# Kernel tuning notes

Hardware: AMD Instinct MI355X
Metric: run time of the kernel (lower is better)

The kernel has to match this reference:

```python
import jax, jax.numpy as jnp
import numpy as np

NEG_INF = float(np.finfo(np.float32).min)
B, KLEN, QLEN, KDIM, QDIM, ADIM, H = 2, 2048, 2048, 512, 512, 512, 8
D_K = ADIM // H


def setup_inputs() -> dict:
    key = jax.random.key(0)
    ks = jax.random.split(key, 12)
    s = 0.05  # param init scale
    inp = {
        "key_in": jax.random.normal(ks[0], (B, KLEN, KDIM), jnp.float32),
        "value_in": jax.random.normal(ks[1], (B, KLEN, KDIM), jnp.float32),
        "query_in": jax.random.normal(ks[2], (B, QLEN, QDIM), jnp.float32),
        "Wk": jax.random.normal(ks[3], (KDIM, ADIM), jnp.float32) * s,
        "bk": jax.random.normal(ks[4], (ADIM,), jnp.float32) * s,
        "Wv": jax.random.normal(ks[5], (KDIM, ADIM), jnp.float32) * s,
        "bv": jax.random.normal(ks[6], (ADIM,), jnp.float32) * s,
        "Wq": jax.random.normal(ks[7], (QDIM, ADIM), jnp.float32) * s,
        "bq": jax.random.normal(ks[8], (ADIM,), jnp.float32) * s,
        "Wo": jax.random.normal(ks[9], (ADIM, KDIM), jnp.float32) * s,
        "bo": jax.random.normal(ks[10], (KDIM,), jnp.float32) * s,
    }
    # key-length padding mask, [B, qlen, klen]; 0 = masked
    klens = jnp.array([KLEN, KLEN - 512], jnp.int32)
    valid = (jnp.arange(KLEN)[None, :] < klens[:, None]).astype(jnp.int32)  # [B, klen]
    inp["mask"] = jnp.broadcast_to(valid[:, None, :], (B, QLEN, KLEN))
    return inp


def reference(key_in, value_in, query_in, Wk, bk, Wv, bv, Wq, bq, Wo, bo, mask):
    # projections -> [B, L, H, d_k]
    k = (key_in @ Wk + bk).reshape(B, KLEN, H, D_K)
    v = (value_in @ Wv + bv).reshape(B, KLEN, H, D_K)
    q = (query_in @ Wq + bq).reshape(B, QLEN, H, D_K)
    # scaled dot-product scores [B, H, qlen, klen]
    e = jnp.einsum('bqhd,bkhd->bhqk', q, k) / jnp.sqrt(jnp.float32(D_K))
    e = jnp.where(mask[:, None, :, :] == 0, NEG_INF, e)
    aw = jax.nn.softmax(e, axis=-1)  # dropout p=0.0 -> identity
    cv = jnp.einsum('bhqk,bkhd->bqhd', aw, v).reshape(B, QLEN, ADIM)
    cv = cv @ Wo + bo  # [B, qlen, kdim]
    return cv, aw
```

## Files before the change

kernel.cpp:

```cpp
#include <hip/hip_runtime.h>

typedef short sh8 __attribute__((ext_vector_type(8)));
typedef float fx4 __attribute__((ext_vector_type(4)));
typedef float fl4 __attribute__((ext_vector_type(4)));
typedef unsigned short us4 __attribute__((ext_vector_type(4)));

__device__ __forceinline__ unsigned short f2bf(float f) {
    union { float f; unsigned u; } v; v.f = f;
    unsigned r = v.u + 0x7FFFu + ((v.u >> 16) & 1u);
    return (unsigned short)(r >> 16);
}
__device__ __forceinline__ float EX2(float x) { return __builtin_amdgcn_exp2f(x); }
__device__ __forceinline__ unsigned cvtpk(float a, float b) {
    unsigned r;
    asm("v_cvt_pk_bf16_f32 %0, %1, %2" : "=v"(r) : "v"(a), "v"(b));
    return r;
}
__device__ __forceinline__ void gl16(const unsigned short* g, unsigned short* l) {
    __builtin_amdgcn_global_load_lds(
        (const __attribute__((address_space(1))) unsigned int*)g,
        (__attribute__((address_space(3))) unsigned int*)l, 16, 0, 0);
}

__global__ __launch_bounds__(256) void prep(const float* __restrict__ x0,
                                            const float* __restrict__ x1,
                                            const float* __restrict__ x2,
                                            const float* __restrict__ w0,
                                            const float* __restrict__ w1,
                                            const float* __restrict__ w2,
                                            const float* __restrict__ w3,
                                            const int* __restrict__ mask,
                                            unsigned short* __restrict__ in_bf,
                                            unsigned short* __restrict__ wt,
                                            unsigned long long* __restrict__ mp2) {
    __shared__ float tw[32][33];
    const int bid = blockIdx.x, tid = threadIdx.x;
    if (bid < 1536) {
        const int z = bid >> 9, xb = bid & 511;
        const float* src = z == 0 ? x0 : (z == 1 ? x1 : x2);
        unsigned short* dst = in_bf + (size_t)z * 2097152;
        for (int i = xb * 256 + tid; i < 524288; i += 131072) {
            float4 v = ((const float4*)src)[i];
            ushort4 o;
            o.x = f2bf(v.x); o.y = f2bf(v.y); o.z = f2bf(v.z); o.w = f2bf(v.w);
            ((ushort4*)dst)[i] = o;
        }
    } else if (bid < 2560) {
        const int t = bid - 1536;
        const int z = t >> 8, bx = t & 15, by = (t >> 4) & 15;
        const float* W = z == 0 ? w0 : z == 1 ? w1 : z == 2 ? w2 : w3;
        unsigned short* Wt = wt + (size_t)z * 262144;
        const int tx = tid & 31, ty = tid >> 5;
        #pragma unroll
        for (int i = 0; i < 4; ++i)
            tw[ty + i * 8][tx] = W[(size_t)(by * 32 + ty + i * 8) * 512 + bx * 32 + tx];
        __syncthreads();
        #pragma unroll
        for (int i = 0; i < 4; ++i)
            Wt[(size_t)(bx * 32 + ty + i * 8) * 512 + by * 32 + tx] = f2bf(tw[tx][ty + i * 8]);
    } else {
        const int p = bid - 2560;
        const int b = p >> 3, k = (p & 7) * 256 + tid;
        int v = mask[(size_t)b * 4194304 + k];
        unsigned long long bal = __ballot(v != 0);
        if ((tid & 63) == 0) mp2[b * 32 + (k >> 6)] = bal;
    }
}

template <int MODE>
__global__ __launch_bounds__(256) void gemm_k(const unsigned short* __restrict__ Aall,
                                              const unsigned short* __restrict__ Wtall,
                                              const float* __restrict__ b0,
                                              const float* __restrict__ b1,
                                              const float* __restrict__ b2,
                                              void* __restrict__ outp,
                                              unsigned short* __restrict__ VtB) {
    const int z = blockIdx.z;
    const unsigned short* A  = Aall  + (size_t)z * (4096 * 512);
    const unsigned short* Bt = Wtall + (size_t)z * (512 * 512);
    const float* bias = (MODE == 0) ? (z == 0 ? b0 : (z == 1 ? b1 : b2)) : b0;

    __shared__ __align__(16) unsigned short As[128 * 64];
    __shared__ __align__(16) unsigned short Bs[64 * 64];

    const int tid = threadIdx.x;
    const int wid = tid >> 6, lane = tid & 63, lr = lane & 15, lg = lane >> 4;
    const int wr = wid >> 1, wc = wid & 1;
    const int mblk = blockIdx.x * 128, nblk = blockIdx.y * 64;
    const int r7 = lr & 7;

    fx4 acc[4][2];
    #pragma unroll
    for (int mf = 0; mf < 4; ++mf)
        #pragma unroll
        for (int nf = 0; nf < 2; ++nf)
            #pragma unroll
            for (int j = 0; j < 4; ++j) acc[mf][nf][j] = 0.f;

    for (int kt = 0; kt < 8; ++kt) {
        __syncthreads();
        #pragma unroll
        for (int g = 0; g < 4; ++g) {
            int ci = wid * 256 + g * 64 + lane;
            int r = ci >> 3, c = (ci & 7) ^ (r & 7);
            gl16(A + (size_t)(mblk + r) * 512 + kt * 64 + c * 8, &As[(wid * 256 + g * 64) * 8]);
        }
        #pragma unroll
        for (int g = 0; g < 2; ++g) {
            int ci = wid * 128 + g * 64 + lane;
            int r = ci >> 3, c = (ci & 7) ^ (r & 7);
            gl16(Bt + (size_t)(nblk + r) * 512 + kt * 64 + c * 8, &Bs[(wid * 128 + g * 64) * 8]);
        }
        __syncthreads();
        #pragma unroll
        for (int d = 0; d < 2; ++d) {
            sh8 af[4], bf[2];
            #pragma unroll
            for (int mf = 0; mf < 4; ++mf)
                af[mf] = *(const sh8*)&As[(wr * 64 + mf * 16 + lr) * 64 + (((d * 4 + lg) ^ r7) * 8)];
            #pragma unroll
            for (int nf = 0; nf < 2; ++nf)
                bf[nf] = *(const sh8*)&Bs[(wc * 32 + nf * 16 + lr) * 64 + (((d * 4 + lg) ^ r7) * 8)];
            #pragma unroll
            for (int mf = 0; mf < 4; ++mf)
                #pragma unroll
                for (int nf = 0; nf < 2; ++nf)
                    acc[mf][nf] = __builtin_amdgcn_mfma_f32_16x16x32_bf16(af[mf], bf[nf], acc[mf][nf], 0, 0, 0);
        }
    }

    if (MODE == 0 && z == 1) {
        #pragma unroll
        for (int nf = 0; nf < 2; ++nf) {
            int n = nblk + wc * 32 + nf * 16 + lr;
            float bv = bias[n];
            int h = n >> 6, dd = n & 63;
            #pragma unroll
            for (int mf = 0; mf < 4; ++mf) {
                int m0 = mblk + wr * 64 + mf * 16 + lg * 4;
                int bb = m0 >> 11, lq = m0 & 2047;
                ushort4 o;
                o.x = f2bf(acc[mf][nf][0] + bv);
                o.y = f2bf(acc[mf][nf][1] + bv);
                o.z = f2bf(acc[mf][nf][2] + bv);
                o.w = f2bf(acc[mf][nf][3] + bv);
                *(ushort4*)(VtB + ((size_t)(bb * 8 + h) * 64 + dd) * 2048 + lq) = o;
            }
        }
    } else {
        #pragma unroll
        for (int nf = 0; nf < 2; ++nf) {
            int n = nblk + wc * 32 + nf * 16 + lr;
            float bv = bias[n];
            #pragma unroll
            for (int mf = 0; mf < 4; ++mf) {
                #pragma unroll
                for (int j = 0; j < 4; ++j) {
                    int m = mblk + wr * 64 + mf * 16 + lg * 4 + j;
                    float val = acc[mf][nf][j] + bv;
                    if (MODE == 0) {
                        if (z == 2) val *= 0.180336880f;
                        int bb = m >> 11, lq = m & 2047, h = n >> 6, dd = n & 63;
                        ((unsigned short*)outp)[(size_t)(((z * 2 + bb) * 8 + h) * 2048 + lq) * 64 + dd] = f2bf(val);
                    } else {
                        ((float*)outp)[(size_t)m * 512 + n] = val;
                    }
                }
            }
        }
    }
}

__device__ __forceinline__ void stage_k1(const unsigned short* Kg, unsigned short* sK,
                                         int t, int w, int lane) {
    #pragma unroll
    for (int g = 0; g < 2; ++g) {
        int ci = w * 128 + g * 64 + lane;
        int r = ci >> 3, c = (ci & 7) ^ (r & 7);
        gl16(Kg + (size_t)(t * 64 + r) * 64 + c * 8, sK + (w * 128 + g * 64) * 8);
    }
}
__device__ __forceinline__ void stage_kv(const unsigned short* Kg, const unsigned short* Vg,
                                         unsigned short* sK, unsigned short* sV,
                                         int t, int w, int lane) {
    #pragma unroll
    for (int g = 0; g < 2; ++g) {
        int ci = w * 128 + g * 64 + lane;
        int r = ci >> 3, c = (ci & 7) ^ (r & 7);
        gl16(Kg + (size_t)(t * 64 + r) * 64 + c * 8, sK + (w * 128 + g * 64) * 8);
        gl16(Vg + (size_t)r * 2048 + t * 64 + c * 8, sV + (w * 128 + g * 64) * 8);
    }
}

__global__ __launch_bounds__(256, 2) void attn_fused(const unsigned short* __restrict__ qkv,
                                                     const unsigned short* __restrict__ Vt,
                                                     const unsigned long long* __restrict__ mp2,
                                                     float* __restrict__ aw,
                                                     unsigned short* __restrict__ cv) {
    const int bid = blockIdx.x;
    const int swz = (bid & 7) * 64 + (bid >> 3);
    const int qb = swz & 31, bh = swz >> 5;
    const int b = bh >> 3, h = bh & 7;
    const unsigned short* Kg = qkv + (size_t)bh * 131072;
    const unsigned short* Vg = Vt + (size_t)bh * 131072;
    const unsigned short* Qg = qkv + 2 * 2097152 + (size_t)bh * 131072 + (size_t)qb * 4096;

    __shared__ __align__(16) unsigned short Ks[2][4096];
    __shared__ __align__(16) unsigned short Vs[2][4096];
    __shared__ __align__(16) unsigned short Pb[4096];

    const int tid = threadIdx.x, w = tid >> 6, lane = tid & 63, lr = lane & 15, lg = lane >> 4;
    const int r7 = lr & 7;
    const int q = qb * 64 + w * 16 + lr;

    sh8 qf0 = *(const sh8*)(Qg + (w * 16 + lr) * 64 + lg * 8);
    sh8 qf1 = *(const sh8*)(Qg + (w * 16 + lr) * 64 + 32 + lg * 8);
    unsigned long long mwv = (lane < 32) ? mp2[b * 32 + lane] : 0ull;

    float m_ = -3e38f, l_ = 0.f;
    asm volatile("s_waitcnt vmcnt(0)" ::: "memory");
    stage_k1(Kg, Ks[0], 0, w, lane);
    stage_k1(Kg, Ks[1], 1, w, lane);
    for (int kt = 0; kt < 32; ++kt) {
        if (kt >= 1 && kt <= 30)
            stage_k1(Kg, Ks[(kt + 1) & 1], kt + 1, w, lane);
        if (kt == 31) asm volatile("s_waitcnt vmcnt(0)" ::: "memory");
        else          asm volatile("s_waitcnt vmcnt(2)" ::: "memory");
        asm volatile("s_barrier" ::: "memory");
        unsigned long long mw = __shfl(mwv, kt, 64);
        if (mw != 0ull) {
            const unsigned short* KsB = Ks[kt & 1];
            fx4 accs[4];
            #pragma unroll
            for (int mt = 0; mt < 4; ++mt) {
                sh8 kf0 = *(const sh8*)&KsB[(mt * 16 + lr) * 64 + ((lg ^ r7) * 8)];
                sh8 kf1 = *(const sh8*)&KsB[(mt * 16 + lr) * 64 + (((4 + lg) ^ r7) * 8)];
                fx4 zz; zz[0] = 0.f; zz[1] = 0.f; zz[2] = 0.f; zz[3] = 0.f;
                zz = __builtin_amdgcn_mfma_f32_16x16x32_bf16(kf0, qf0, zz, 0, 0, 0);
                accs[mt] = __builtin_amdgcn_mfma_f32_16x16x32_bf16(kf1, qf1, zz, 0, 0, 0);
            }
            float sv[16], tmax = -3e38f;
            if (mw == ~0ull) {
                #pragma unroll
                for (int mt = 0; mt < 4; ++mt)
                    #pragma unroll
                    for (int j = 0; j < 4; ++j) {
                        float s = accs[mt][j];
                        sv[mt * 4 + j] = s; tmax = fmaxf(tmax, s);
                    }
            } else {
                #pragma unroll
                for (int mt = 0; mt < 4; ++mt)
                    #pragma unroll
                    for (int j = 0; j < 4; ++j) {
                        int kl = mt * 16 + lg * 4 + j;
                        bool ok = (mw >> kl) & 1ull;
                        float s = ok ? accs[mt][j] : -3e38f;
                        sv[mt * 4 + j] = s; tmax = fmaxf(tmax, s);
                    }
            }
            float mnew = fmaxf(m_, tmax);
            float ps = 0.f;
            #pragma unroll
            for (int i = 0; i < 16; ++i) ps += EX2(sv[i] - mnew);
            l_ = l_ * EX2(m_ - mnew) + ps;
            m_ = mnew;
        }
        asm volatile("s_barrier" ::: "memory");
    }
    #pragma unroll
    for (int off = 16; off <= 32; off <<= 1) {
        float mo = __shfl_xor(m_, off), lo = __shfl_xor(l_, off);
        float mn = fmaxf(m_, mo);
        l_ = l_ * EX2(m_ - mn) + lo * EX2(mo - mn);
        m_ = mn;
    }
    const float Mshift = (l_ > 0.f) ? (m_ + __log2f(l_)) : 3e38f;

    fx4 acco[4];
    #pragma unroll
    for (int md = 0; md < 4; ++md) { acco[md][0] = 0.f; acco[md][1] = 0.f; acco[md][2] = 0.f; acco[md][3] = 0.f; }
    float* awb = aw + (size_t)bh * 4194304 + (size_t)q * 2048;

    asm volatile("s_waitcnt vmcnt(0)" ::: "memory");
    stage_kv(Kg, Vg, Ks[0], Vs[0], 0, w, lane);
    stage_kv(Kg, Vg, Ks[1], Vs[1], 1, w, lane);

    for (int kt = 0; kt < 32; ++kt) {
        if (kt >= 1 && kt <= 30)
            stage_kv(Kg, Vg, Ks[(kt + 1) & 1], Vs[(kt + 1) & 1], kt + 1, w, lane);
        if (kt == 0 || kt == 31) asm volatile("s_waitcnt vmcnt(4)" ::: "memory");
        else                     asm volatile("s_waitcnt vmcnt(8)" ::: "memory");
        asm volatile("s_barrier" ::: "memory");

        unsigned long long mw = __shfl(mwv, kt, 64);
        const unsigned short* KsB = Ks[kt & 1];
        const unsigned short* VsB = Vs[kt & 1];

        if (mw != 0ull) {
            fx4 accs[4];
            #pragma unroll
            for (int mt = 0; mt < 4; ++mt) {
                sh8 kf0 = *(const sh8*)&KsB[(mt * 16 + lr) * 64 + ((lg ^ r7) * 8)];
                sh8 kf1 = *(const sh8*)&KsB[(mt * 16 + lr) * 64 + (((4 + lg) ^ r7) * 8)];
                fx4 zz; zz[0] = 0.f; zz[1] = 0.f; zz[2] = 0.f; zz[3] = 0.f;
                zz = __builtin_amdgcn_mfma_f32_16x16x32_bf16(kf0, qf0, zz, 0, 0, 0);
                accs[mt] = __builtin_amdgcn_mfma_f32_16x16x32_bf16(kf1, qf1, zz, 0, 0, 0);
            }
            bool full = (mw == ~0ull);
            #pragma unroll
            for (int mt = 0; mt < 4; ++mt) {
                fl4 pw;
                #pragma unroll
                for (int j = 0; j < 4; ++j) {
                    int kl = mt * 16 + lg * 4 + j;
                    bool ok = full || ((mw >> kl) & 1ull);
                    pw[j] = EX2((ok ? accs[mt][j] : -3e38f) - Mshift);
                }
                *(fl4*)(awb + kt * 64 + mt * 16 + lg * 4) = pw;
                int sc = (mt * 2 + (lg >> 1)) ^ r7;
                *(uint2*)&Pb[(w * 16 + lr) * 64 + sc * 8 + (lg & 1) * 4] =
                    make_uint2(cvtpk(pw[0], pw[1]), cvtpk(pw[2], pw[3]));
            }
            asm volatile("s_waitcnt lgkmcnt(0)" ::: "memory");
            __builtin_amdgcn_sched_barrier(0);
            sh8 bp0 = *(const sh8*)&Pb[(w * 16 + lr) * 64 + ((lg ^ r7) * 8)];
            sh8 bp1 = *(const sh8*)&Pb[(w * 16 + lr) * 64 + (((4 + lg) ^ r7) * 8)];
            #pragma unroll
            for (int md = 0; md < 4; ++md) {
                sh8 vf0 = *(const sh8*)&VsB[(md * 16 + lr) * 64 + ((lg ^ r7) * 8)];
                sh8 vf1 = *(const sh8*)&VsB[(md * 16 + lr) * 64 + (((4 + lg) ^ r7) * 8)];
                acco[md] = __builtin_amdgcn_mfma_f32_16x16x32_bf16(vf0, bp0, acco[md], 0, 0, 0);
                acco[md] = __builtin_amdgcn_mfma_f32_16x16x32_bf16(vf1, bp1, acco[md], 0, 0, 0);
            }
        } else {
            fl4 z4 = {0.f, 0.f, 0.f, 0.f};
            #pragma unroll
            for (int mt = 0; mt < 4; ++mt)
                *(fl4*)(awb + kt * 64 + mt * 16 + lg * 4) = z4;
        }
        asm volatile("s_barrier" ::: "memory");
    }

    #pragma unroll
    for (int md = 0; md < 4; ++md) {
        uint2 o = make_uint2(cvtpk(acco[md][0], acco[md][1]), cvtpk(acco[md][2], acco[md][3]));
        *(uint2*)(cv + (size_t)(b * 2048 + q) * 512 + h * 64 + md * 16 + lg * 4) = o;
    }
}

extern "C" void kernel_launch(void* const* d_in, const int* in_sizes, int n_in,
                              void* d_out, int out_size, void* d_ws, size_t ws_size,
                              hipStream_t stream) {
    const float* key_in   = (const float*)d_in[0];
    const float* value_in = (const float*)d_in[1];
    const float* query_in = (const float*)d_in[2];
    const float* Wk = (const float*)d_in[3];
    const float* bk = (const float*)d_in[4];
    const float* Wv = (const float*)d_in[5];
    const float* bv = (const float*)d_in[6];
    const float* Wq = (const float*)d_in[7];
    const float* bq = (const float*)d_in[8];
    const float* Wo = (const float*)d_in[9];
    const float* bo = (const float*)d_in[10];
    const int* mask = (const int*)d_in[11];

    char* ws = (char*)d_ws;
    unsigned short* in_bf = (unsigned short*)(ws);
    unsigned short* qkv   = (unsigned short*)(ws + 12582912);
    unsigned short* cvb   = (unsigned short*)(ws + 12582912 + 4194304);
    unsigned short* wt    = (unsigned short*)(ws + 25165824);
    unsigned short* VtB   = (unsigned short*)(ws + 27262976);
    unsigned long long* mp2 = (unsigned long long*)(ws + 31457280);

    float* out_cv = (float*)d_out;
    float* out_aw = (float*)d_out + 2097152;

    prep<<<dim3(2576), 256, 0, stream>>>(key_in, value_in, query_in,
                                         Wk, Wv, Wq, Wo, mask, in_bf, wt, mp2);
    gemm_k<0><<<dim3(32, 8, 3), 256, 0, stream>>>(in_bf, wt, bk, bv, bq, qkv, VtB);
    attn_fused<<<dim3(512), 256, 0, stream>>>(qkv, VtB, mp2, out_aw, cvb);
    gemm_k<1><<<dim3(32, 8, 1), 256, 0, stream>>>(cvb, wt + 3 * 262144, bo, bo, bo, out_cv, (unsigned short*)nullptr);
}
```

Before: 123.9 us.

## Split softmax statistics pass into separate split-K kernel before attention pass

Measured after the change: 172.3 us. 1.39x slower.

```diff
diff --git a/kernel.cpp b/kernel.cpp
--- a/kernel.cpp
+++ b/kernel.cpp
@@ -171,15 +171,81 @@
     }
 }
 
-__device__ __forceinline__ void stage_k1(const unsigned short* Kg, unsigned short* sK,
-                                         int t, int w, int lane) {
-    #pragma unroll
-    for (int g = 0; g < 2; ++g) {
-        int ci = w * 128 + g * 64 + lane;
-        int r = ci >> 3, c = (ci & 7) ^ (r & 7);
-        gl16(Kg + (size_t)(t * 64 + r) * 64 + c * 8, sK + (w * 128 + g * 64) * 8);
-    }
-}
+__global__ __launch_bounds__(256) void attn_stats(const unsigned short* __restrict__ qkv,
+                                                  const unsigned long long* __restrict__ mp2,
+                                                  float2* __restrict__ sp) {
+    const int bid = blockIdx.x;
+    const int swz = (bid & 7) * 256 + (bid >> 3);
+    const int qb = swz & 31, bh = (swz >> 5) & 15, ks = swz >> 9;
+    const int b = bh >> 3;
+    const unsigned short* Kg = qkv + (size_t)bh * 131072 + (size_t)ks * 512 * 64;
+    const unsigned short* Qg = qkv + 2 * 2097152 + (size_t)bh * 131072 + (size_t)qb * 4096;
+    const int tid = threadIdx.x, w = tid >> 6, lane = tid & 63, lr = lane & 15, lg = lane >> 4;
+    float2* spo = sp + (size_t)ks * 32768 + bh * 2048 + qb * 64;
+
+    unsigned long long mws[8];
+    bool any = false;
+    #pragma unroll
+    for (int kt = 0; kt < 8; ++kt) { mws[kt] = mp2[b * 32 + ks * 8 + kt]; any |= (mws[kt] != 0ull); }
+    if (!any) {
+        if (tid < 64) spo[tid] = make_float2(-3e38f, 0.f);
+        return;
+    }
+
+    sh8 qf0 = *(const sh8*)(Qg + (w * 16 + lr) * 64 + lg * 8);
+    sh8 qf1 = *(const sh8*)(Qg + (w * 16 + lr) * 64 + 32 + lg * 8);
+
+    float m_ = -3e38f, l_ = 0.f;
+    for (int kt = 0; kt < 8; ++kt) {
+        unsigned long long mw = mws[kt];
+        if (mw == 0ull) continue;
+        const unsigned short* Kt = Kg + kt * 4096;
+        fx4 accs[4];
+        #pragma unroll
+        for (int mt = 0; mt < 4; ++mt) {
+            sh8 kf0 = *(const sh8*)(Kt + (mt * 16 + lr) * 64 + lg * 8);
+            sh8 kf1 = *(const sh8*)(Kt + (mt * 16 + lr) * 64 + 32 + lg * 8);
+            fx4 zz; zz[0] = 0.f; zz[1] = 0.f; zz[2] = 0.f; zz[3] = 0.f;
+            zz = __builtin_amdgcn_mfma_f32_16x16x32_bf16(kf0, qf0, zz, 0, 0, 0);
+            accs[mt] = __builtin_amdgcn_mfma_f32_16x16x32_bf16(kf1, qf1, zz, 0, 0, 0);
+        }
+        float sv[16], tmax = -3e38f;
+        if (mw == ~0ull) {
+            #pragma unroll
+            for (int mt = 0; mt < 4; ++mt)
+                #pragma unroll
+                for (int j = 0; j < 4; ++j) {
+                    float s = accs[mt][j];
+                    sv[mt * 4 + j] = s; tmax = fmaxf(tmax, s);
+                }
+        } else {
+            #pragma unroll
+            for (int mt = 0; mt < 4; ++mt)
+                #pragma unroll
+                for (int j = 0; j < 4; ++j) {
+                    int kl = mt * 16 + lg * 4 + j;
+                    bool ok = (mw >> kl) & 1ull;
+                    float s = ok ? accs[mt][j] : -3e38f;
+                    sv[mt * 4 + j] = s; tmax = fmaxf(tmax, s);
+                }
+        }
+        float mnew = fmaxf(m_, tmax);
+        float ps = 0.f;
+        #pragma unroll
+        for (int i = 0; i < 16; ++i) ps += EX2(sv[i] - mnew);
+        l_ = l_ * EX2(m_ - mnew) + ps;
+        m_ = mnew;
+    }
+    #pragma unroll
+    for (int off = 16; off <= 32; off <<= 1) {
+        float mo = __shfl_xor(m_, off), lo = __shfl_xor(l_, off);
+        float mn = fmaxf(m_, mo);
+        l_ = l_ * EX2(m_ - mn) + lo * EX2(mo - mn);
+        m_ = mn;
+    }
+    if (lg == 0) spo[w * 16 + lr] = make_float2(m_, l_);
+}
+
 __device__ __forceinline__ void stage_kv(const unsigned short* Kg, const unsigned short* Vg,
                                          unsigned short* sK, unsigned short* sV,
                                          int t, int w, int lane) {
@@ -192,9 +258,10 @@
     }
 }
 
-__global__ __launch_bounds__(256, 2) void attn_fused(const unsigned short* __restrict__ qkv,
+__global__ __launch_bounds__(256, 2) void attn_pass2(const unsigned short* __restrict__ qkv,
                                                      const unsigned short* __restrict__ Vt,
                                                      const unsigned long long* __restrict__ mp2,
+                                                     const float2* __restrict__ sp,
                                                      float* __restrict__ aw,
                                                      unsigned short* __restrict__ cv) {
     const int bid = blockIdx.x;
@@ -213,69 +280,18 @@
     const int r7 = lr & 7;
     const int q = qb * 64 + w * 16 + lr;
 
+    float mm = -3e38f;
+    float2 vv[4];
+    #pragma unroll
+    for (int s4 = 0; s4 < 4; ++s4) { vv[s4] = sp[(size_t)s4 * 32768 + bh * 2048 + q]; mm = fmaxf(mm, vv[s4].x); }
+    float ll = 0.f;
+    #pragma unroll
+    for (int s4 = 0; s4 < 4; ++s4) ll += vv[s4].y * EX2(vv[s4].x - mm);
+    const float Mshift = (ll > 0.f) ? (mm + __log2f(ll)) : 3e38f;
+
     sh8 qf0 = *(const sh8*)(Qg + (w * 16 + lr) * 64 + lg * 8);
     sh8 qf1 = *(const sh8*)(Qg + (w * 16 + lr) * 64 + 32 + lg * 8);
     unsigned long long mwv = (lane < 32) ? mp2[b * 32 + lane] : 0ull;
-
-    float m_ = -3e38f, l_ = 0.f;
-    asm volatile("s_waitcnt vmcnt(0)" ::: "memory");
-    stage_k1(Kg, Ks[0], 0, w, lane);
-    stage_k1(Kg, Ks[1], 1, w, lane);
-    for (int kt = 0; kt < 32; ++kt) {
-        if (kt >= 1 && kt <= 30)
-            stage_k1(Kg, Ks[(kt + 1) & 1], kt + 1, w, lane);
-        if (kt == 31) asm volatile("s_waitcnt vmcnt(0)" ::: "memory");
-        else          asm volatile("s_waitcnt vmcnt(2)" ::: "memory");
-        asm volatile("s_barrier" ::: "memory");
-        unsigned long long mw = __shfl(mwv, kt, 64);
-        if (mw != 0ull) {
-            const unsigned short* KsB = Ks[kt & 1];
-            fx4 accs[4];
-            #pragma unroll
-            for (int mt = 0; mt < 4; ++mt) {
-                sh8 kf0 = *(const sh8*)&KsB[(mt * 16 + lr) * 64 + ((lg ^ r7) * 8)];
-                sh8 kf1 = *(const sh8*)&KsB[(mt * 16 + lr) * 64 + (((4 + lg) ^ r7) * 8)];
-                fx4 zz; zz[0] = 0.f; zz[1] = 0.f; zz[2] = 0.f; zz[3] = 0.f;
-                zz = __builtin_amdgcn_mfma_f32_16x16x32_bf16(kf0, qf0, zz, 0, 0, 0);
-                accs[mt] = __builtin_amdgcn_mfma_f32_16x16x32_bf16(kf1, qf1, zz, 0, 0, 0);
-            }
-            float sv[16], tmax = -3e38f;
-            if (mw == ~0ull) {
-                #pragma unroll
-                for (int mt = 0; mt < 4; ++mt)
-                    #pragma unroll
-                    for (int j = 0; j < 4; ++j) {
-                        float s = accs[mt][j];
-                        sv[mt * 4 + j] = s; tmax = fmaxf(tmax, s);
-                    }
-            } else {
-                #pragma unroll
-                for (int mt = 0; mt < 4; ++mt)
-                    #pragma unroll
-                    for (int j = 0; j < 4; ++j) {
-                        int kl = mt * 16 + lg * 4 + j;
-                        bool ok = (mw >> kl) & 1ull;
-                        float s = ok ? accs[mt][j] : -3e38f;
-                        sv[mt * 4 + j] = s; tmax = fmaxf(tmax, s);
-                    }
-            }
-            float mnew = fmaxf(m_, tmax);
-            float ps = 0.f;
-            #pragma unroll
-            for (int i = 0; i < 16; ++i) ps += EX2(sv[i] - mnew);
-            l_ = l_ * EX2(m_ - mnew) + ps;
-            m_ = mnew;
-        }
-        asm volatile("s_barrier" ::: "memory");
-    }
-    #pragma unroll
-    for (int off = 16; off <= 32; off <<= 1) {
-        float mo = __shfl_xor(m_, off), lo = __shfl_xor(l_, off);
-        float mn = fmaxf(m_, mo);
-        l_ = l_ * EX2(m_ - mn) + lo * EX2(mo - mn);
-        m_ = mn;
-    }
-    const float Mshift = (l_ > 0.f) ? (m_ + __log2f(l_)) : 3e38f;
 
     fx4 acco[4];
     #pragma unroll
@@ -372,6 +388,7 @@
     unsigned short* wt    = (unsigned short*)(ws + 25165824);
     unsigned short* VtB   = (unsigned short*)(ws + 27262976);
     unsigned long long* mp2 = (unsigned long long*)(ws + 31457280);
+    float2*         sp    = (float2*)(ws + 31458304);
 
     float* out_cv = (float*)d_out;
     float* out_aw = (float*)d_out + 2097152;
@@ -379,6 +396,7 @@
     prep<<<dim3(2576), 256, 0, stream>>>(key_in, value_in, query_in,
                                          Wk, Wv, Wq, Wo, mask, in_bf, wt, mp2);
     gemm_k<0><<<dim3(32, 8, 3), 256, 0, stream>>>(in_bf, wt, bk, bv, bq, qkv, VtB);
-    attn_fused<<<dim3(512), 256, 0, stream>>>(qkv, VtB, mp2, out_aw, cvb);
+    attn_stats<<<dim3(2048), 256, 0, stream>>>(qkv, mp2, sp);
+    attn_pass2<<<dim3(512), 256, 0, stream>>>(qkv, VtB, mp2, sp, out_aw, cvb);
     gemm_k<1><<<dim3(32, 8, 1), 256, 0, stream>>>(cvb, wt + 3 * 262144, bo, bo, bo, out_cv, (unsigned short*)nullptr);
 }
```

## Deepen K prefetch ring in stats pass and use nontemporal stores for weights

Applied to the files above, without the earlier changes.

Result: slower. 133.6 us (+7.8%).

```diff
diff --git a/kernel.cpp b/kernel.cpp
--- a/kernel.cpp
+++ b/kernel.cpp
@@ -205,8 +205,7 @@
     const unsigned short* Vg = Vt + (size_t)bh * 131072;
     const unsigned short* Qg = qkv + 2 * 2097152 + (size_t)bh * 131072 + (size_t)qb * 4096;
 
-    __shared__ __align__(16) unsigned short Ks[2][4096];
-    __shared__ __align__(16) unsigned short Vs[2][4096];
+    __shared__ __align__(16) unsigned short KR[4][4096];
     __shared__ __align__(16) unsigned short Pb[4096];
 
     const int tid = threadIdx.x, w = tid >> 6, lane = tid & 63, lr = lane & 15, lg = lane >> 4;
@@ -219,17 +218,20 @@
 
     float m_ = -3e38f, l_ = 0.f;
     asm volatile("s_waitcnt vmcnt(0)" ::: "memory");
-    stage_k1(Kg, Ks[0], 0, w, lane);
-    stage_k1(Kg, Ks[1], 1, w, lane);
-    for (int kt = 0; kt < 32; ++kt) {
-        if (kt >= 1 && kt <= 30)
-            stage_k1(Kg, Ks[(kt + 1) & 1], kt + 1, w, lane);
-        if (kt == 31) asm volatile("s_waitcnt vmcnt(0)" ::: "memory");
-        else          asm volatile("s_waitcnt vmcnt(2)" ::: "memory");
+    stage_k1(Kg, KR[0], 0, w, lane);
+    stage_k1(Kg, KR[1], 1, w, lane);
+    stage_k1(Kg, KR[2], 2, w, lane);
+    stage_k1(Kg, KR[3], 3, w, lane);
+    for (int p = 0; p < 16; ++p) {
+        if (p == 15) asm volatile("s_waitcnt vmcnt(0)" ::: "memory");
+        else         asm volatile("s_waitcnt vmcnt(4)" ::: "memory");
         asm volatile("s_barrier" ::: "memory");
-        unsigned long long mw = __shfl(mwv, kt, 64);
-        if (mw != 0ull) {
-            const unsigned short* KsB = Ks[kt & 1];
+        #pragma unroll
+        for (int tt = 0; tt < 2; ++tt) {
+            const int kt = p * 2 + tt;
+            unsigned long long mw = __shfl(mwv, kt, 64);
+            if (mw == 0ull) continue;
+            const unsigned short* KsB = KR[0] + (kt & 3) * 4096;
             fx4 accs[4];
             #pragma unroll
             for (int mt = 0; mt < 4; ++mt) {
@@ -267,6 +269,10 @@
             m_ = mnew;
         }
         asm volatile("s_barrier" ::: "memory");
+        if (p < 14) {
+            stage_k1(Kg, KR[0] + ((p * 2) & 3) * 4096, p * 2 + 4, w, lane);
+            stage_k1(Kg, KR[0] + ((p * 2 + 1) & 3) * 4096, p * 2 + 5, w, lane);
+        }
     }
     #pragma unroll
     for (int off = 16; off <= 32; off <<= 1) {
@@ -277,25 +283,28 @@
     }
     const float Mshift = (l_ > 0.f) ? (m_ + __log2f(l_)) : 3e38f;
 
+    unsigned short* Ks0 = KR[0];
+    unsigned short* Vs0 = KR[2];
     fx4 acco[4];
     #pragma unroll
     for (int md = 0; md < 4; ++md) { acco[md][0] = 0.f; acco[md][1] = 0.f; acco[md][2] = 0.f; acco[md][3] = 0.f; }
     float* awb = aw + (size_t)bh * 4194304 + (size_t)q * 2048;
 
     asm volatile("s_waitcnt vmcnt(0)" ::: "memory");
-    stage_kv(Kg, Vg, Ks[0], Vs[0], 0, w, lane);
-    stage_kv(Kg, Vg, Ks[1], Vs[1], 1, w, lane);
+    stage_kv(Kg, Vg, Ks0, Vs0, 0, w, lane);
+    stage_kv(Kg, Vg, Ks0 + 4096, Vs0 + 4096, 1, w, lane);
 
     for (int kt = 0; kt < 32; ++kt) {
         if (kt >= 1 && kt <= 30)
-            stage_kv(Kg, Vg, Ks[(kt + 1) & 1], Vs[(kt + 1) & 1], kt + 1, w, lane);
+            stage_kv(Kg, Vg, Ks0 + ((kt + 1) & 1) * 4096, Vs0 + ((kt + 1) & 1) * 4096,
+                     kt + 1, w, lane);
         if (kt == 0 || kt == 31) asm volatile("s_waitcnt vmcnt(4)" ::: "memory");
         else                     asm volatile("s_waitcnt vmcnt(8)" ::: "memory");
         asm volatile("s_barrier" ::: "memory");
 
         unsigned long long mw = __shfl(mwv, kt, 64);
-        const unsigned short* KsB = Ks[kt & 1];
-        const unsigned short* VsB = Vs[kt & 1];
+        const unsigned short* KsB = Ks0 + (kt & 1) * 4096;
+        const unsigned short* VsB = Vs0 + (kt & 1) * 4096;
 
         if (mw != 0ull) {
             fx4 accs[4];
@@ -317,7 +326,7 @@
                     bool ok = full || ((mw >> kl) & 1ull);
                     pw[j] = EX2((ok ? accs[mt][j] : -3e38f) - Mshift);
                 }
-                *(fl4*)(awb + kt * 64 + mt * 16 + lg * 4) = pw;
+                __builtin_nontemporal_store(pw, (fl4*)(awb + kt * 64 + mt * 16 + lg * 4));
                 int sc = (mt * 2 + (lg >> 1)) ^ r7;
                 *(uint2*)&Pb[(w * 16 + lr) * 64 + sc * 8 + (lg & 1) * 4] =
                     make_uint2(cvtpk(pw[0], pw[1]), cvtpk(pw[2], pw[3]));
@@ -337,7 +346,7 @@
             fl4 z4 = {0.f, 0.f, 0.f, 0.f};
             #pragma unroll
             for (int mt = 0; mt < 4; ++mt)
-                *(fl4*)(awb + kt * 64 + mt * 16 + lg * 4) = z4;
+                __builtin_nontemporal_store(z4, (fl4*)(awb + kt * 64 + mt * 16 + lg * 4));
         }
         asm volatile("s_barrier" ::: "memory");
     }
```
